# Performance work log

Measured on AMD Instinct MI355X. Metric: run time of the kernel, lower is better.

## Reference

```python
import jax, jax.numpy as jnp
import numpy as np

B, T, A, H = 2048, 512, 32, 16


def setup_inputs() -> dict:
    key = jax.random.key(0)
    ks = jax.random.split(key, 10)
    s = 1.0 / np.sqrt(H)
    inputs = jax.random.normal(ks[0], (B, T, A), dtype=jnp.float32)
    masks = (jax.random.uniform(ks[1], (B, T)) > 0.05).astype(jnp.float32)
    h0 = jnp.zeros((1, B, H), dtype=jnp.float32)
    c0 = jnp.zeros((1, B, H), dtype=jnp.float32)
    # torch nn.LSTM params (gate order i,f,g,o) and linear heads
    w_ih = jax.random.uniform(ks[2], (4 * H, A), minval=-s, maxval=s)
    w_hh = jax.random.uniform(ks[3], (4 * H, H), minval=-s, maxval=s)
    b_ih = jax.random.uniform(ks[4], (4 * H,), minval=-s, maxval=s)
    b_hh = jax.random.uniform(ks[5], (4 * H,), minval=-s, maxval=s)
    w_actor = jax.random.uniform(ks[6], (A, H), minval=-s, maxval=s)
    b_actor = jax.random.uniform(ks[7], (A,), minval=-s, maxval=s)
    w_critic = jax.random.uniform(ks[8], (1, H), minval=-s, maxval=s)
    b_critic = jax.random.uniform(ks[9], (1,), minval=-s, maxval=s)
    return {"inputs": inputs, "masks": masks, "h0": h0, "c0": c0,
            "w_ih": w_ih, "w_hh": w_hh, "b_ih": b_ih, "b_hh": b_hh,
            "w_actor": w_actor, "b_actor": b_actor,
            "w_critic": w_critic, "b_critic": b_critic}


def reference(inputs, masks, h0, c0, w_ih, w_hh, b_ih, b_hh,
              w_actor, b_actor, w_critic, b_critic):
    # masked LSTM scan: state is zeroed where mask==0 before each step
    def step(carry, xm):
        h, c = carry                      # [B,H]
        x, m = xm                         # x:[B,A], m:[B]
        h = h * m[:, None]
        c = c * m[:, None]
        gates = x @ w_ih.T + b_ih + h @ w_hh.T + b_hh   # [B,4H]
        i, f, g, o = jnp.split(gates, 4, axis=-1)
        i = jax.nn.sigmoid(i)
        f = jax.nn.sigmoid(f)
        g = jnp.tanh(g)
        o = jax.nn.sigmoid(o)
        c2 = f * c + i * g
        h2 = o * jnp.tanh(c2)
        return (h2, c2), h2

    xs = (jnp.swapaxes(inputs, 0, 1), masks.T)          # time-major
    (hT, cT), feats = jax.lax.scan(step, (h0[0], c0[0]), xs)
    feats = jnp.swapaxes(feats, 0, 1)                   # [B,T,H]
    actor = feats @ w_actor.T + b_actor                 # [B,T,A]
    critic = feats @ w_critic.T + b_critic              # [B,T,1]
    return actor, critic, hT[None], cT[None]
```

## Files before the change

kernel.cpp:

```cpp
#include <hip/hip_runtime.h>
#include <stdint.h>

#define Bn 2048
#define Tn 512
#define An 32
#define Hn 16

typedef __attribute__((ext_vector_type(8))) short bf16x8;
typedef __attribute__((ext_vector_type(4))) float f32x4;

union FragU { bf16x8 v; uint32_t u[4]; };

static __device__ __forceinline__ uint32_t pack_hi16(float a, float b){
  return (__float_as_uint(b) & 0xFFFF0000u) | (__float_as_uint(a) >> 16);
}
static __device__ __forceinline__ void split8(const float* s, FragU& hi, FragU& lo){
#pragma unroll
  for (int d = 0; d < 4; ++d){
    float a = s[2*d], b = s[2*d+1];
    float ah = __uint_as_float(__float_as_uint(a) & 0xFFFF0000u);
    float bh = __uint_as_float(__float_as_uint(b) & 0xFFFF0000u);
    hi.u[d] = pack_hi16(a, b);
    lo.u[d] = pack_hi16(a - ah, b - bh);
  }
}
static __device__ __forceinline__ uint32_t plo(uint32_t e, uint32_t o){
  return __builtin_amdgcn_perm(o, e, 0x05040100u);
}
static __device__ __forceinline__ f32x4 MF(const FragU& a, const FragU& b, f32x4 c){
  return __builtin_amdgcn_mfma_f32_16x16x32_bf16(a.v, b.v, c, 0, 0, 0);
}
static __device__ __forceinline__ void buildBHh(const uint32_t* pk, int srcA, int srcB,
                                                FragU& BHh){
  uint32_t d0 = (uint32_t)__builtin_amdgcn_ds_bpermute(srcA, (int)pk[0]);
  uint32_t d1 = (uint32_t)__builtin_amdgcn_ds_bpermute(srcA, (int)pk[1]);
  uint32_t d2 = (uint32_t)__builtin_amdgcn_ds_bpermute(srcA, (int)pk[2]);
  uint32_t d3 = (uint32_t)__builtin_amdgcn_ds_bpermute(srcA, (int)pk[3]);
  uint32_t d4 = (uint32_t)__builtin_amdgcn_ds_bpermute(srcB, (int)pk[0]);
  uint32_t d5 = (uint32_t)__builtin_amdgcn_ds_bpermute(srcB, (int)pk[1]);
  uint32_t d6 = (uint32_t)__builtin_amdgcn_ds_bpermute(srcB, (int)pk[2]);
  uint32_t d7 = (uint32_t)__builtin_amdgcn_ds_bpermute(srcB, (int)pk[3]);
  BHh.u[0] = plo(d0, d1); BHh.u[1] = plo(d2, d3);
  BHh.u[2] = plo(d4, d5); BHh.u[3] = plo(d6, d7);
}

__global__ __launch_bounds__(64, 1)
void lstm_fused(const float* __restrict__ xin,
                const float* __restrict__ masks,
                const float* __restrict__ h0,
                const float* __restrict__ c0,
                const float* __restrict__ w_ih,
                const float* __restrict__ w_hh,
                const float* __restrict__ b_ih,
                const float* __restrict__ b_hh,
                const float* __restrict__ w_act,
                const float* __restrict__ b_act,
                const float* __restrict__ w_cr,
                const float* __restrict__ b_cr,
                float* __restrict__ actor,
                float* __restrict__ critic,
                float* __restrict__ hT,
                float* __restrict__ cT)
{
  const int l = threadIdx.x;
  const int q = l >> 4;
  const int n = l & 15;
  const int b0 = blockIdx.x * 16;
  const int colbase = (q & 1) * 8;

  const float KS = -1.44269504088896f;
  const float KG =  2.88539008177793f;

  FragU wihH0, wihL0, whhA0; f32x4 bias0;
  FragU wihH1, wihL1, whhA1; f32x4 bias1;
  FragU wihH2, wihL2, whhA2; f32x4 bias2;
  FragU wihH3, wihL3, whhA3; f32x4 bias3;
  {
    auto loadGate = [&](int g, float sc, FragU& wh, FragU& wl, FragU& a1, f32x4& bg){
      float tmp[8];
#pragma unroll
      for (int j = 0; j < 8; ++j) tmp[j] = w_ih[(g*16 + n)*32 + q*8 + j] * sc;
      split8(tmp, wh, wl);
#pragma unroll
      for (int j = 0; j < 8; ++j) tmp[j] = w_hh[(g*16 + n)*16 + colbase + j] * sc;
      FragU hh, hl; split8(tmp, hh, hl);
#pragma unroll
      for (int d = 0; d < 4; ++d)
        a1.u[d] = (q < 2) ? hh.u[d] : hl.u[d];
#pragma unroll
      for (int r = 0; r < 4; ++r)
        bg[r] = (b_ih[g*16 + q*4 + r] + b_hh[g*16 + q*4 + r]) * sc;
    };
    loadGate(0, KS, wihH0, wihL0, whhA0, bias0);
    loadGate(1, KS, wihH1, wihL1, whhA1, bias1);
    loadGate(2, KG, wihH2, wihL2, whhA2, bias2);
    loadGate(3, KS, wihH3, wihL3, whhA3, bias3);
  }
  FragU whA0, whA1f, wcA;
  f32x4 biasA0, biasA1;
  const float bcr = b_cr[0];
  {
    float tmp[8];
#pragma unroll
    for (int j = 0; j < 8; ++j) tmp[j] = w_act[(0*16 + n)*16 + colbase + j];
    { FragU hh, hl; split8(tmp, hh, hl);
#pragma unroll
      for (int d = 0; d < 4; ++d) whA0.u[d] = (q < 2) ? hh.u[d] : hl.u[d]; }
#pragma unroll
    for (int r = 0; r < 4; ++r) biasA0[r] = b_act[0*16 + q*4 + r];
#pragma unroll
    for (int j = 0; j < 8; ++j) tmp[j] = w_act[(1*16 + n)*16 + colbase + j];
    { FragU hh, hl; split8(tmp, hh, hl);
#pragma unroll
      for (int d = 0; d < 4; ++d) whA1f.u[d] = (q < 2) ? hh.u[d] : hl.u[d]; }
#pragma unroll
    for (int r = 0; r < 4; ++r) biasA1[r] = b_act[1*16 + q*4 + r];
#pragma unroll
    for (int j = 0; j < 8; ++j) tmp[j] = (n == 0) ? w_cr[colbase + j] : 0.0f;
    { FragU hh, hl; split8(tmp, hh, hl);
#pragma unroll
      for (int d = 0; d < 4; ++d) wcA.u[d] = (q < 2) ? hh.u[d] : hl.u[d]; }
  }

  const int srcA = (((q & 1) * 2) * 16 + n) * 4;
  const int srcB = srcA + 64;

  float cs[4], hs[4];
#pragma unroll
  for (int r = 0; r < 4; ++r){
    hs[r] = h0[(b0 + n)*16 + q*4 + r];
    cs[r] = c0[(b0 + n)*16 + q*4 + r];
  }
  uint32_t pk[4];
#pragma unroll
  for (int r = 0; r < 4; ++r) pk[r] = __float_as_uint(hs[r]) >> 16;
  FragU BHh;
  buildBHh(pk, srcA, srcB, BHh);

  const f32x4 zero4 = {0.f, 0.f, 0.f, 0.f};

  const size_t xrow = (size_t)(b0 + n) * Tn * 32 + q * 8;
  float4 xA[4], xB[4];
#pragma unroll
  for (int u = 0; u < 4; ++u){
    xA[u] = *(const float4*)&xin[xrow + (size_t)u * 32];
    xB[u] = *(const float4*)&xin[xrow + (size_t)u * 32 + 4];
  }
  const size_t mrow = (size_t)(b0 + n) * Tn;
  float4 mQ = *(const float4*)&masks[mrow];

  for (int t0 = 0; t0 < Tn; t0 += 4){
    const int tb = (t0 + 4 < Tn) ? (t0 + 4) : 0;
    float4 mN = *(const float4*)&masks[mrow + tb];
#pragma unroll
    for (int u = 0; u < 4; ++u){
      const int t = t0 + u;
      const float m = (u == 0) ? mQ.x : (u == 1) ? mQ.y : (u == 2) ? mQ.z : mQ.w;

      FragU Xh, Xl;
      {
        float s[8] = {xA[u].x, xA[u].y, xA[u].z, xA[u].w,
                      xB[u].x, xB[u].y, xB[u].z, xB[u].w};
        split8(s, Xh, Xl);
      }
      {
        const int tn = (t + 4 < Tn) ? (t + 4) : t;
        xA[u] = *(const float4*)&xin[xrow + (size_t)tn * 32];
        xB[u] = *(const float4*)&xin[xrow + (size_t)tn * 32 + 4];
      }

      f32x4 ax0 = MF(wihH0, Xh, bias0); ax0 = MF(wihH0, Xl, ax0); ax0 = MF(wihL0, Xh, ax0);
      f32x4 ax1 = MF(wihH1, Xh, bias1); ax1 = MF(wihH1, Xl, ax1); ax1 = MF(wihL1, Xh, ax1);
      f32x4 ax2 = MF(wihH2, Xh, bias2); ax2 = MF(wihH2, Xl, ax2); ax2 = MF(wihL2, Xh, ax2);
      f32x4 ax3 = MF(wihH3, Xh, bias3); ax3 = MF(wihH3, Xl, ax3);

      f32x4 ah0 = MF(whhA0, BHh, zero4);
      f32x4 ah1 = MF(whhA1, BHh, zero4);
      f32x4 ah2 = MF(whhA2, BHh, zero4);
      f32x4 ah3 = MF(whhA3, BHh, zero4);

      if (t){
        const int th = t - 1;
        f32x4 a0 = MF(whA0, BHh, biasA0);
        __builtin_nontemporal_store(a0,
            (f32x4*)&actor[((size_t)(b0 + n) * Tn + th) * 32 + 0*16 + q*4]);
        f32x4 a1 = MF(whA1f, BHh, biasA1);
        __builtin_nontemporal_store(a1,
            (f32x4*)&actor[((size_t)(b0 + n) * Tn + th) * 32 + 1*16 + q*4]);
        f32x4 cc = MF(wcA, BHh, zero4);
        if (q == 0)
          __builtin_nontemporal_store(cc[0] + bcr,
              &critic[(size_t)(b0 + n) * Tn + th]);
      }

#pragma unroll
      for (int r = 0; r < 4; ++r){
        float gi = ax0[r] + m * ah0[r];
        float gf = ax1[r] + m * ah1[r];
        float gg = ax2[r] + m * ah2[r];
        float go = ax3[r] + m * ah3[r];
        float iv = __builtin_amdgcn_rcpf(1.0f + __builtin_amdgcn_exp2f(gi));
        float fv = __builtin_amdgcn_rcpf(1.0f + __builtin_amdgcn_exp2f(gf));
        float gr = __builtin_amdgcn_rcpf(1.0f + __builtin_amdgcn_exp2f(gg));
        float ov = __builtin_amdgcn_rcpf(1.0f + __builtin_amdgcn_exp2f(go));
        float gv = 1.0f - 2.0f * gr;
        float c2 = fv * (cs[r] * m) + iv * gv;
        float et = __builtin_amdgcn_rcpf(1.0f + __builtin_amdgcn_exp2f(c2 * KG));
        float h2 = ov - 2.0f * (ov * et);
        cs[r] = c2;
        hs[r] = h2;
        pk[r] = __float_as_uint(h2) >> 16;
      }
      buildBHh(pk, srcA, srcB, BHh);
    }
    mQ = mN;
  }

  {
    const int th = Tn - 1;
    f32x4 a0 = MF(whA0, BHh, biasA0);
    __builtin_nontemporal_store(a0,
        (f32x4*)&actor[((size_t)(b0 + n) * Tn + th) * 32 + 0*16 + q*4]);
    f32x4 a1 = MF(whA1f, BHh, biasA1);
    __builtin_nontemporal_store(a1,
        (f32x4*)&actor[((size_t)(b0 + n) * Tn + th) * 32 + 1*16 + q*4]);
    f32x4 cc = MF(wcA, BHh, zero4);
    if (q == 0)
      __builtin_nontemporal_store(cc[0] + bcr, &critic[(size_t)(b0 + n) * Tn + th]);
  }
  *(float4*)&hT[(b0 + n)*16 + q*4] = make_float4(hs[0], hs[1], hs[2], hs[3]);
  *(float4*)&cT[(b0 + n)*16 + q*4] = make_float4(cs[0], cs[1], cs[2], cs[3]);
}

extern "C" void kernel_launch(void* const* d_in, const int* in_sizes, int n_in,
                              void* d_out, int out_size, void* d_ws, size_t ws_size,
                              hipStream_t stream) {
  (void)in_sizes; (void)n_in; (void)out_size; (void)d_ws; (void)ws_size;
  const float* xin   = (const float*)d_in[0];
  const float* masks = (const float*)d_in[1];
  const float* h0    = (const float*)d_in[2];
  const float* c0    = (const float*)d_in[3];
  const float* w_ih  = (const float*)d_in[4];
  const float* w_hh  = (const float*)d_in[5];
  const float* b_ih  = (const float*)d_in[6];
  const float* b_hh  = (const float*)d_in[7];
  const float* w_act = (const float*)d_in[8];
  const float* b_act = (const float*)d_in[9];
  const float* w_cr  = (const float*)d_in[10];
  const float* b_cr  = (const float*)d_in[11];

  float* out    = (float*)d_out;
  float* actor  = out;
  float* critic = out + (size_t)Bn * Tn * An;
  float* hT     = critic + (size_t)Bn * Tn;
  float* cT     = hT + (size_t)Bn * Hn;

  lstm_fused<<<Bn/16, 64, 0, stream>>>(xin, masks, h0, c0, w_ih, w_hh, b_ih, b_hh,
                                       w_act, b_act, w_cr, b_cr,
                                       actor, critic, hT, cT);
}
```

Baseline: 480.8 us.

## Split sequences at episode resets and schedule segments sorted by length

Result: slower. 866.6 us (+80.2%).

```diff
diff --git a/kernel.cpp b/kernel.cpp
--- a/kernel.cpp
+++ b/kernel.cpp
@@ -5,6 +5,11 @@
 #define Tn 512
 #define An 32
 #define Hn 16
+
+#define SEG_CAP 131072
+#define WS_HIST 8
+#define WS_CURS 1024
+#define WS_SSEG 4096
 
 typedef __attribute__((ext_vector_type(8))) short bf16x8;
 typedef __attribute__((ext_vector_type(4))) float f32x4;
@@ -44,28 +49,65 @@
   BHh.u[2] = plo(d4, d5); BHh.u[3] = plo(d6, d7);
 }
 
-__global__ __launch_bounds__(64, 1)
-void lstm_fused(const float* __restrict__ xin,
-                const float* __restrict__ masks,
-                const float* __restrict__ h0,
-                const float* __restrict__ c0,
-                const float* __restrict__ w_ih,
-                const float* __restrict__ w_hh,
-                const float* __restrict__ b_ih,
-                const float* __restrict__ b_hh,
-                const float* __restrict__ w_act,
-                const float* __restrict__ b_act,
-                const float* __restrict__ w_cr,
-                const float* __restrict__ b_cr,
-                float* __restrict__ actor,
-                float* __restrict__ critic,
-                float* __restrict__ hT,
-                float* __restrict__ cT)
+
+__global__ void seg_count(const float* __restrict__ masks, uint32_t* __restrict__ ws){
+  int row = blockIdx.x * 64 + threadIdx.x;
+  if (row >= Bn) return;
+  const float* mr = &masks[(size_t)row * Tn];
+  int prev = 0;
+  for (int t = 1; t < Tn; ++t){
+    if (mr[t] == 0.0f){ atomicAdd(&ws[WS_HIST + (t - prev)], 1u); prev = t; }
+  }
+  atomicAdd(&ws[WS_HIST + (Tn - prev)], 1u);
+}
+
+__global__ void seg_offsets(uint32_t* __restrict__ ws){
+  const int l = threadIdx.x;
+  uint32_t h[8]; uint32_t s = 0;
+#pragma unroll
+  for (int j = 0; j < 8; ++j){ int len = 512 - (l*8 + j); h[j] = ws[WS_HIST + len]; s += h[j]; }
+  uint32_t v = s;
+  for (int d = 1; d < 64; d <<= 1){ uint32_t t = __shfl_up(v, d); if (l >= d) v += t; }
+  uint32_t run = v - s;
+#pragma unroll
+  for (int j = 0; j < 8; ++j){ int len = 512 - (l*8 + j); ws[WS_CURS + len] = run; run += h[j]; }
+  if (l == 63){ ws[2] = run; ws[1] = (run + 15u) >> 4; }
+}
+
+__global__ void seg_place(const float* __restrict__ masks, uint32_t* __restrict__ ws){
+  int row = blockIdx.x * 64 + threadIdx.x;
+  if (row >= Bn) return;
+  const float* mr = &masks[(size_t)row * Tn];
+  int prev = 0;
+  for (int t = 1; t < Tn; ++t){
+    if (mr[t] == 0.0f){
+      int len = t - prev;
+      uint32_t idx = atomicAdd(&ws[WS_CURS + len], 1u);
+      if (idx < SEG_CAP)
+        ws[WS_SSEG + idx] = ((uint32_t)row << 19) | ((uint32_t)prev << 10) | (uint32_t)len;
+      prev = t;
+    }
+  }
+  int len = Tn - prev;
+  uint32_t idx = atomicAdd(&ws[WS_CURS + len], 1u);
+  if (idx < SEG_CAP)
+    ws[WS_SSEG + idx] = ((uint32_t)row << 19) | ((uint32_t)prev << 10) | (uint32_t)len;
+}
+
+__global__ __launch_bounds__(64, 2)
+void lstm_seg(const float* __restrict__ xin, const float* __restrict__ masks,
+              const float* __restrict__ h0, const float* __restrict__ c0,
+              const float* __restrict__ w_ih, const float* __restrict__ w_hh,
+              const float* __restrict__ b_ih, const float* __restrict__ b_hh,
+              const float* __restrict__ w_act, const float* __restrict__ b_act,
+              const float* __restrict__ w_cr, const float* __restrict__ b_cr,
+              float* __restrict__ actor, float* __restrict__ critic,
+              float* __restrict__ hT, float* __restrict__ cT,
+              const uint32_t* __restrict__ ws)
 {
   const int l = threadIdx.x;
   const int q = l >> 4;
   const int n = l & 15;
-  const int b0 = blockIdx.x * 16;
   const int colbase = (q & 1) * 8;
 
   const float KS = -1.44269504088896f;
@@ -85,8 +127,7 @@
       for (int j = 0; j < 8; ++j) tmp[j] = w_hh[(g*16 + n)*16 + colbase + j] * sc;
       FragU hh, hl; split8(tmp, hh, hl);
 #pragma unroll
-      for (int d = 0; d < 4; ++d)
-        a1.u[d] = (q < 2) ? hh.u[d] : hl.u[d];
+      for (int d = 0; d < 4; ++d) a1.u[d] = (q < 2) ? hh.u[d] : hl.u[d];
 #pragma unroll
       for (int r = 0; r < 4; ++r)
         bg[r] = (b_ih[g*16 + q*4 + r] + b_hh[g*16 + q*4 + r]) * sc;
@@ -124,6 +165,208 @@
 
   const int srcA = (((q & 1) * 2) * 16 + n) * 4;
   const int srcB = srcA + 64;
+  const f32x4 zero4 = {0.f, 0.f, 0.f, 0.f};
+
+  const uint32_t nseg = ws[2];
+  const uint32_t nb   = ws[1];
+  const uint32_t* sseg = &ws[WS_SSEG];
+
+  for (uint32_t b = blockIdx.x; b < nb; b += gridDim.x){
+    const uint32_t idx = b * 16u + (uint32_t)n;
+    const uint32_t sv = (idx < nseg) ? sseg[idx] : 0u;
+    const int srow = (int)(sv >> 19);
+    const int st0  = (int)((sv >> 10) & 0x1FFu);
+    const int slen = (int)(sv & 0x3FFu);
+    int ml = slen;
+    { int o;
+      o = __shfl_xor(ml, 1); ml = ml > o ? ml : o;
+      o = __shfl_xor(ml, 2); ml = ml > o ? ml : o;
+      o = __shfl_xor(ml, 4); ml = ml > o ? ml : o;
+      o = __shfl_xor(ml, 8); ml = ml > o ? ml : o; }
+    if (ml == 0) continue;
+    const int lm1 = (slen > 0) ? (slen - 1) : 0;
+
+    float cs[4], hs[4];
+    {
+      const float m0 = masks[(size_t)srow * Tn];
+      const bool z = (st0 == 0);
+#pragma unroll
+      for (int r = 0; r < 4; ++r){
+        float hv = h0[srow*16 + q*4 + r] * m0;
+        float cv = c0[srow*16 + q*4 + r] * m0;
+        hs[r] = z ? hv : 0.f;
+        cs[r] = z ? cv : 0.f;
+      }
+    }
+    uint32_t pk[4];
+#pragma unroll
+    for (int r = 0; r < 4; ++r) pk[r] = __float_as_uint(hs[r]) >> 16;
+    FragU BHh;
+    buildBHh(pk, srcA, srcB, BHh);
+
+    const size_t xbase = ((size_t)srow * Tn + st0) * 32 + q * 8;
+    const size_t obase = (size_t)srow * Tn + st0;
+
+    float4 xA[4], xB[4];
+#pragma unroll
+    for (int u = 0; u < 4; ++u){
+      int sc = u < lm1 ? u : lm1;
+      const float* p = &xin[xbase + (size_t)sc * 32];
+      xA[u] = *(const float4*)p;
+      xB[u] = *(const float4*)(p + 4);
+    }
+
+    for (int s0 = 0; s0 < ml; s0 += 4){
+#pragma unroll
+      for (int u = 0; u < 4; ++u){
+        const int s = s0 + u;
+
+        FragU Xh, Xl;
+        {
+          float sarr[8] = {xA[u].x, xA[u].y, xA[u].z, xA[u].w,
+                           xB[u].x, xB[u].y, xB[u].z, xB[u].w};
+          split8(sarr, Xh, Xl);
+        }
+        {
+          int sc = (s + 4) < lm1 ? (s + 4) : lm1;
+          const float* p = &xin[xbase + (size_t)sc * 32];
+          xA[u] = *(const float4*)p;
+          xB[u] = *(const float4*)(p + 4);
+        }
+
+        f32x4 ax0 = MF(wihH0, Xh, bias0); ax0 = MF(wihH0, Xl, ax0); ax0 = MF(wihL0, Xh, ax0);
+        f32x4 ax1 = MF(wihH1, Xh, bias1); ax1 = MF(wihH1, Xl, ax1); ax1 = MF(wihL1, Xh, ax1);
+        f32x4 ax2 = MF(wihH2, Xh, bias2); ax2 = MF(wihH2, Xl, ax2); ax2 = MF(wihL2, Xh, ax2);
+        f32x4 ax3 = MF(wihH3, Xh, bias3); ax3 = MF(wihH3, Xl, ax3);
+
+        f32x4 ah0 = MF(whhA0, BHh, zero4);
+        f32x4 ah1 = MF(whhA1, BHh, zero4);
+        f32x4 ah2 = MF(whhA2, BHh, zero4);
+        f32x4 ah3 = MF(whhA3, BHh, zero4);
+
+        if (s){
+          f32x4 a0 = MF(whA0, BHh, biasA0);
+          f32x4 a1 = MF(whA1f, BHh, biasA1);
+          f32x4 cc = MF(wcA, BHh, zero4);
+          if (s - 1 < slen){
+            *(f32x4*)&actor[(obase + (s - 1)) * 32 + q*4]      = a0;
+            *(f32x4*)&actor[(obase + (s - 1)) * 32 + 16 + q*4] = a1;
+            if (q == 0) critic[obase + (s - 1)] = cc[0] + bcr;
+          }
+        }
+
+        const bool act = (s < slen);
+#pragma unroll
+        for (int r = 0; r < 4; ++r){
+          float gi = ax0[r] + ah0[r];
+          float gf = ax1[r] + ah1[r];
+          float gg = ax2[r] + ah2[r];
+          float go = ax3[r] + ah3[r];
+          float iv = __builtin_amdgcn_rcpf(1.0f + __builtin_amdgcn_exp2f(gi));
+          float fv = __builtin_amdgcn_rcpf(1.0f + __builtin_amdgcn_exp2f(gf));
+          float gr = __builtin_amdgcn_rcpf(1.0f + __builtin_amdgcn_exp2f(gg));
+          float ov = __builtin_amdgcn_rcpf(1.0f + __builtin_amdgcn_exp2f(go));
+          float gv = 1.0f - 2.0f * gr;
+          float c2 = fv * cs[r] + iv * gv;
+          float et = __builtin_amdgcn_rcpf(1.0f + __builtin_amdgcn_exp2f(c2 * KG));
+          float h2 = ov - 2.0f * (ov * et);
+          cs[r] = act ? c2 : cs[r];
+          hs[r] = act ? h2 : hs[r];
+          pk[r] = __float_as_uint(hs[r]) >> 16;
+        }
+        buildBHh(pk, srcA, srcB, BHh);
+      }
+    }
+
+    if ((ml & 3) == 0){
+      f32x4 a0 = MF(whA0, BHh, biasA0);
+      f32x4 a1 = MF(whA1f, BHh, biasA1);
+      f32x4 cc = MF(wcA, BHh, zero4);
+      if (slen == ml){
+        *(f32x4*)&actor[(obase + (ml - 1)) * 32 + q*4]      = a0;
+        *(f32x4*)&actor[(obase + (ml - 1)) * 32 + 16 + q*4] = a1;
+        if (q == 0) critic[obase + (ml - 1)] = cc[0] + bcr;
+      }
+    }
+
+    if (slen > 0 && st0 + slen == Tn){
+      *(float4*)&hT[srow*16 + q*4] = make_float4(hs[0], hs[1], hs[2], hs[3]);
+      *(float4*)&cT[srow*16 + q*4] = make_float4(cs[0], cs[1], cs[2], cs[3]);
+    }
+  }
+}
+
+__global__ __launch_bounds__(64, 1)
+void lstm_fused(const float* __restrict__ xin, const float* __restrict__ masks,
+                const float* __restrict__ h0, const float* __restrict__ c0,
+                const float* __restrict__ w_ih, const float* __restrict__ w_hh,
+                const float* __restrict__ b_ih, const float* __restrict__ b_hh,
+                const float* __restrict__ w_act, const float* __restrict__ b_act,
+                const float* __restrict__ w_cr, const float* __restrict__ b_cr,
+                float* __restrict__ actor, float* __restrict__ critic,
+                float* __restrict__ hT, float* __restrict__ cT)
+{
+  const int l = threadIdx.x;
+  const int q = l >> 4;
+  const int n = l & 15;
+  const int b0 = blockIdx.x * 16;
+  const int colbase = (q & 1) * 8;
+
+  const float KS = -1.44269504088896f;
+  const float KG =  2.88539008177793f;
+
+  FragU wihH0, wihL0, whhA0; f32x4 bias0;
+  FragU wihH1, wihL1, whhA1; f32x4 bias1;
+  FragU wihH2, wihL2, whhA2; f32x4 bias2;
+  FragU wihH3, wihL3, whhA3; f32x4 bias3;
+  {
+    auto loadGate = [&](int g, float sc, FragU& wh, FragU& wl, FragU& a1, f32x4& bg){
+      float tmp[8];
+#pragma unroll
+      for (int j = 0; j < 8; ++j) tmp[j] = w_ih[(g*16 + n)*32 + q*8 + j] * sc;
+      split8(tmp, wh, wl);
+#pragma unroll
+      for (int j = 0; j < 8; ++j) tmp[j] = w_hh[(g*16 + n)*16 + colbase + j] * sc;
+      FragU hh, hl; split8(tmp, hh, hl);
+#pragma unroll
+      for (int d = 0; d < 4; ++d) a1.u[d] = (q < 2) ? hh.u[d] : hl.u[d];
+#pragma unroll
+      for (int r = 0; r < 4; ++r)
+        bg[r] = (b_ih[g*16 + q*4 + r] + b_hh[g*16 + q*4 + r]) * sc;
+    };
+    loadGate(0, KS, wihH0, wihL0, whhA0, bias0);
+    loadGate(1, KS, wihH1, wihL1, whhA1, bias1);
+    loadGate(2, KG, wihH2, wihL2, whhA2, bias2);
+    loadGate(3, KS, wihH3, wihL3, whhA3, bias3);
+  }
+  FragU whA0, whA1f, wcA;
+  f32x4 biasA0, biasA1;
+  const float bcr = b_cr[0];
+  {
+    float tmp[8];
+#pragma unroll
+    for (int j = 0; j < 8; ++j) tmp[j] = w_act[(0*16 + n)*16 + colbase + j];
+    { FragU hh, hl; split8(tmp, hh, hl);
+#pragma unroll
+      for (int d = 0; d < 4; ++d) whA0.u[d] = (q < 2) ? hh.u[d] : hl.u[d]; }
+#pragma unroll
+    for (int r = 0; r < 4; ++r) biasA0[r] = b_act[0*16 + q*4 + r];
+#pragma unroll
+    for (int j = 0; j < 8; ++j) tmp[j] = w_act[(1*16 + n)*16 + colbase + j];
+    { FragU hh, hl; split8(tmp, hh, hl);
+#pragma unroll
+      for (int d = 0; d < 4; ++d) whA1f.u[d] = (q < 2) ? hh.u[d] : hl.u[d]; }
+#pragma unroll
+    for (int r = 0; r < 4; ++r) biasA1[r] = b_act[1*16 + q*4 + r];
+#pragma unroll
+    for (int j = 0; j < 8; ++j) tmp[j] = (n == 0) ? w_cr[colbase + j] : 0.0f;
+    { FragU hh, hl; split8(tmp, hh, hl);
+#pragma unroll
+      for (int d = 0; d < 4; ++d) wcA.u[d] = (q < 2) ? hh.u[d] : hl.u[d]; }
+  }
+
+  const int srcA = (((q & 1) * 2) * 16 + n) * 4;
+  const int srcB = srcA + 64;
 
   float cs[4], hs[4];
 #pragma unroll
@@ -138,7 +381,6 @@
   buildBHh(pk, srcA, srcB, BHh);
 
   const f32x4 zero4 = {0.f, 0.f, 0.f, 0.f};
-
   const size_t xrow = (size_t)(b0 + n) * Tn * 32 + q * 8;
   float4 xA[4], xB[4];
 #pragma unroll
@@ -156,7 +398,6 @@
     for (int u = 0; u < 4; ++u){
       const int t = t0 + u;
       const float m = (u == 0) ? mQ.x : (u == 1) ? mQ.y : (u == 2) ? mQ.z : mQ.w;
-
       FragU Xh, Xl;
       {
         float s[8] = {xA[u].x, xA[u].y, xA[u].z, xA[u].w,
@@ -168,31 +409,23 @@
         xA[u] = *(const float4*)&xin[xrow + (size_t)tn * 32];
         xB[u] = *(const float4*)&xin[xrow + (size_t)tn * 32 + 4];
       }
-
       f32x4 ax0 = MF(wihH0, Xh, bias0); ax0 = MF(wihH0, Xl, ax0); ax0 = MF(wihL0, Xh, ax0);
       f32x4 ax1 = MF(wihH1, Xh, bias1); ax1 = MF(wihH1, Xl, ax1); ax1 = MF(wihL1, Xh, ax1);
       f32x4 ax2 = MF(wihH2, Xh, bias2); ax2 = MF(wihH2, Xl, ax2); ax2 = MF(wihL2, Xh, ax2);
       f32x4 ax3 = MF(wihH3, Xh, bias3); ax3 = MF(wihH3, Xl, ax3);
-
       f32x4 ah0 = MF(whhA0, BHh, zero4);
       f32x4 ah1 = MF(whhA1, BHh, zero4);
       f32x4 ah2 = MF(whhA2, BHh, zero4);
       f32x4 ah3 = MF(whhA3, BHh, zero4);
-
       if (t){
         const int th = t - 1;
         f32x4 a0 = MF(whA0, BHh, biasA0);
-        __builtin_nontemporal_store(a0,
-            (f32x4*)&actor[((size_t)(b0 + n) * Tn + th) * 32 + 0*16 + q*4]);
+        *(f32x4*)&actor[((size_t)(b0 + n) * Tn + th) * 32 + q*4] = a0;
         f32x4 a1 = MF(whA1f, BHh, biasA1);
-        __builtin_nontemporal_store(a1,
-            (f32x4*)&actor[((size_t)(b0 + n) * Tn + th) * 32 + 1*16 + q*4]);
+        *(f32x4*)&actor[((size_t)(b0 + n) * Tn + th) * 32 + 16 + q*4] = a1;
         f32x4 cc = MF(wcA, BHh, zero4);
-        if (q == 0)
-          __builtin_nontemporal_store(cc[0] + bcr,
-              &critic[(size_t)(b0 + n) * Tn + th]);
-      }
-
+        if (q == 0) critic[(size_t)(b0 + n) * Tn + th] = cc[0] + bcr;
+      }
 #pragma unroll
       for (int r = 0; r < 4; ++r){
         float gi = ax0[r] + m * ah0[r];
@@ -215,18 +448,14 @@
     }
     mQ = mN;
   }
-
   {
     const int th = Tn - 1;
     f32x4 a0 = MF(whA0, BHh, biasA0);
-    __builtin_nontemporal_store(a0,
-        (f32x4*)&actor[((size_t)(b0 + n) * Tn + th) * 32 + 0*16 + q*4]);
+    *(f32x4*)&actor[((size_t)(b0 + n) * Tn + th) * 32 + q*4] = a0;
     f32x4 a1 = MF(whA1f, BHh, biasA1);
-    __builtin_nontemporal_store(a1,
-        (f32x4*)&actor[((size_t)(b0 + n) * Tn + th) * 32 + 1*16 + q*4]);
+    *(f32x4*)&actor[((size_t)(b0 + n) * Tn + th) * 32 + 16 + q*4] = a1;
     f32x4 cc = MF(wcA, BHh, zero4);
-    if (q == 0)
-      __builtin_nontemporal_store(cc[0] + bcr, &critic[(size_t)(b0 + n) * Tn + th]);
+    if (q == 0) critic[(size_t)(b0 + n) * Tn + th] = cc[0] + bcr;
   }
   *(float4*)&hT[(b0 + n)*16 + q*4] = make_float4(hs[0], hs[1], hs[2], hs[3]);
   *(float4*)&cT[(b0 + n)*16 + q*4] = make_float4(cs[0], cs[1], cs[2], cs[3]);
@@ -235,7 +464,7 @@
 extern "C" void kernel_launch(void* const* d_in, const int* in_sizes, int n_in,
                               void* d_out, int out_size, void* d_ws, size_t ws_size,
                               hipStream_t stream) {
-  (void)in_sizes; (void)n_in; (void)out_size; (void)d_ws; (void)ws_size;
+  (void)in_sizes; (void)n_in; (void)out_size;
   const float* xin   = (const float*)d_in[0];
   const float* masks = (const float*)d_in[1];
   const float* h0    = (const float*)d_in[2];
@@ -255,7 +484,19 @@
   float* hT     = critic + (size_t)Bn * Tn;
   float* cT     = hT + (size_t)Bn * Hn;
 
-  lstm_fused<<<Bn/16, 64, 0, stream>>>(xin, masks, h0, c0, w_ih, w_hh, b_ih, b_hh,
-                                       w_act, b_act, w_cr, b_cr,
-                                       actor, critic, hT, cT);
-}
+  const size_t WS_NEED = (size_t)(WS_SSEG + SEG_CAP) * sizeof(uint32_t);
+  if (d_ws != nullptr && ws_size >= WS_NEED){
+    uint32_t* wsu = (uint32_t*)d_ws;
+    hipMemsetAsync(d_ws, 0, 8192, stream);
+    seg_count  <<<Bn/64, 64, 0, stream>>>(masks, wsu);
+    seg_offsets<<<1,     64, 0, stream>>>(wsu);
+    seg_place  <<<Bn/64, 64, 0, stream>>>(masks, wsu);
+    lstm_seg   <<<2048,  64, 0, stream>>>(xin, masks, h0, c0, w_ih, w_hh, b_ih, b_hh,
+                                          w_act, b_act, w_cr, b_cr,
+                                          actor, critic, hT, cT, wsu);
+  } else {
+    lstm_fused<<<Bn/16, 64, 0, stream>>>(xin, masks, h0, c0, w_ih, w_hh, b_ih, b_hh,
+                                         w_act, b_act, w_cr, b_cr,
+                                         actor, critic, hT, cT);
+  }
+}
```
